# Kernel tuning notes

Hardware: AMD Instinct MI355X
Metric: run time of the kernel (lower is better)

Reference implementation:

```python
import jax, jax.numpy as jnp
import numpy as np

B, V, S, E, K, FF = 16, 512, 1024, 8, 2, 2048  # batch, n_vars, seq_len, n_experts, top_k, ff_dim


def setup_inputs() -> dict:
    key = jax.random.key(0)
    ks = jax.random.split(key, 6)
    def w(k, shape, fan_in):
        return (jax.random.normal(k, shape, jnp.float32) / np.sqrt(fan_in)).astype(jnp.float32)
    return {
        "x": jax.random.normal(ks[0], (B, S, V), jnp.float32),
        "gate_W": w(ks[1], (E, S), S),          # Gating: Linear(seq_len -> n_experts), no bias
        "exp_W": w(ks[2], (E, S, S), S),        # per-expert Linear(seq_len -> seq_len) weights
        "exp_b": jnp.zeros((E, S), jnp.float32),
        "fc1_W": w(ks[3], (FF, V), V),          # MLPFeat fc1: Linear(n_vars -> ff_dim)
        "fc1_b": jnp.zeros((FF,), jnp.float32),
        "fc2_W": w(ks[4], (V, FF), FF),         # MLPFeat fc2: Linear(ff_dim -> n_vars)
        "fc2_b": jnp.zeros((V,), jnp.float32),
    }


def reference(x, gate_W, exp_W, exp_b, fc1_W, fc1_b, fc2_W, fc2_b):
    # Dropout layers are identity at inference.
    res = x                                   # [B,S,V]
    xt = jnp.swapaxes(x, 1, 2)                # [B,V,S] tokens of dim seq_len

    # --- MLPTime (multi_expert MoE) ---
    logits = jnp.einsum('bvs,es->bve', xt, gate_W)      # [B,V,E]
    probs = jax.nn.softmax(logits, axis=-1)             # gate_logits returned by torch code
    w, sel = jax.lax.top_k(probs, K)                    # [B,V,K]
    # combine top-k weights into a dense per-expert weight [B,V,E] (zeros off top-k)
    full_w = jnp.sum(jax.nn.one_hot(sel, E, dtype=xt.dtype) * w[..., None], axis=2)
    # all-expert outputs, then weighted combine (same math as the per-expert scatter loop)
    all_out = jnp.einsum('bvs,eos->bveo', xt, exp_W) + exp_b[None, None]  # [B,V,E,S]
    moe = jnp.einsum('bve,bveo->bvo', full_w, all_out)                    # [B,V,S]
    t = jax.nn.relu(moe)

    x = jnp.swapaxes(t, 1, 2) + res           # [B,S,V] residual

    # --- MLPFeat ---
    res2 = x
    h = jax.nn.relu(x @ fc1_W.T + fc1_b)      # [B,S,FF]
    x = h @ fc2_W.T + fc2_b + res2            # [B,S,V]
    return (x, probs)
```

## Files before the change

kernel.cpp:

```cpp
#include <hip/hip_runtime.h>
#include <stdint.h>

#define B_  16
#define V_  512
#define S_  1024
#define E_  8
#define FF_ 2048
#define NT_ (B_*V_)
#define NR_ (B_*S_)

typedef __attribute__((ext_vector_type(8))) short bf16x8;
typedef __attribute__((ext_vector_type(4))) float f32x4;

__device__ __forceinline__ unsigned short f2bf(float f) {
    unsigned int u = __float_as_uint(f);
    u += 0x7FFFu + ((u >> 16) & 1u);
    return (unsigned short)(u >> 16);
}
__device__ __forceinline__ float bf2f(unsigned short u) {
    return __uint_as_float(((unsigned int)u) << 16);
}

__device__ __forceinline__ void gl_lds16(const void* g, void* l) {
    __builtin_amdgcn_global_load_lds((const __attribute__((address_space(1))) void*)g,
                                     (__attribute__((address_space(3))) void*)l,
                                     16, 0, 0);
}

__device__ __forceinline__ void cvt4(const float* s, unsigned short* d, int i) {
    float4 v = *(const float4*)(s + i);
    ushort4 o; o.x = f2bf(v.x); o.y = f2bf(v.y); o.z = f2bf(v.z); o.w = f2bf(v.w);
    *(ushort4*)(d + i) = o;
}
__global__ void k_convert3(const float* __restrict__ s0, unsigned short* __restrict__ d0, int g0,
                           const float* __restrict__ s1, unsigned short* __restrict__ d1, int g1,
                           const float* __restrict__ s2, unsigned short* __restrict__ d2) {
    int g = blockIdx.x * 256 + threadIdx.x;
    if (g < g0)           cvt4(s0, d0, g * 4);
    else if (g < g0 + g1) cvt4(s1, d1, (g - g0) * 4);
    else                  cvt4(s2, d2, (g - g0 - g1) * 4);
}

__global__ __launch_bounds__(256) void k_xt_gate(const float* __restrict__ x,
                                                 const float* __restrict__ gate_W,
                                                 unsigned short* __restrict__ xt,
                                                 double* __restrict__ part,
                                                 int* __restrict__ cnt) {
    __shared__ float t[32][33];
    __shared__ float gw[E_][128];
    int b = blockIdx.z, sc = blockIdx.y, vt = blockIdx.x;
    int tid = threadIdx.x;
    if (vt == 0 && sc == 0 && b == 0 && tid < E_) cnt[tid] = 0;
    int col = tid & 31, row8 = tid >> 5;
    for (int i = tid; i < E_ * 128; i += 256) {
        int e = i >> 7, j = i & 127;
        gw[e][j] = gate_W[e * S_ + sc * 128 + j];
    }
    double acc = 0.0;
    for (int sub = 0; sub < 4; ++sub) {
        int s0 = sc * 128 + sub * 32;
        __syncthreads();
        for (int r = 0; r < 4; ++r) {
            int sl = row8 + r * 8;
            t[sl][col] = x[(b * S_ + s0 + sl) * V_ + vt * 32 + col];
        }
        __syncthreads();
        for (int r = 0; r < 4; ++r) {
            int vl = row8 + r * 8;
            xt[(size_t)(b * V_ + vt * 32 + vl) * S_ + s0 + col] = f2bf(t[col][vl]);
        }
        #pragma unroll
        for (int s = 0; s < 32; ++s)
            acc += (double)t[s][col] * (double)gw[row8][sub * 32 + s];
    }
    int tok = b * V_ + vt * 32 + col;
    part[((size_t)sc * NT_ + tok) * E_ + row8] = acc;
}

__global__ __launch_bounds__(256) void k_gate_fin(const double* __restrict__ part,
                                                  float* __restrict__ probs_out,
                                                  int* __restrict__ cnt, int* __restrict__ tok_of,
                                                  int* __restrict__ tk_slot, float* __restrict__ tk_w) {
    int t = blockIdx.x * 256 + threadIdx.x;
    int lane = threadIdx.x & 63;
    double l[E_];
    #pragma unroll
    for (int e = 0; e < E_; ++e) l[e] = 0.0;
    for (int c = 0; c < S_ / 128; ++c) {
        const double* p = part + ((size_t)c * NT_ + t) * E_;
        #pragma unroll
        for (int e = 0; e < E_; ++e) l[e] += p[e];
    }
    double m = l[0];
    #pragma unroll
    for (int e = 1; e < E_; ++e) m = l[e] > m ? l[e] : m;
    double p[E_], sum = 0.0;
    #pragma unroll
    for (int e = 0; e < E_; ++e) { p[e] = exp(l[e] - m); sum += p[e]; }
    float pf[E_];
    #pragma unroll
    for (int e = 0; e < E_; ++e) pf[e] = (float)(p[e] / sum);
    float4 pa = {pf[0], pf[1], pf[2], pf[3]}, pb = {pf[4], pf[5], pf[6], pf[7]};
    *(float4*)(probs_out + (size_t)t * E_) = pa;
    *(float4*)(probs_out + (size_t)t * E_ + 4) = pb;
    int i0 = 0;
    #pragma unroll
    for (int e = 1; e < E_; ++e) if (pf[e] > pf[i0]) i0 = e;
    int i1 = -1;
    #pragma unroll
    for (int e = 0; e < E_; ++e) if (e != i0 && (i1 < 0 || pf[e] > pf[i1])) i1 = e;
    int sel[2] = {i0, i1};
    float wsel[2] = {pf[i0], pf[i1]};
    #pragma unroll
    for (int k = 0; k < 2; ++k) {
        int ie = sel[k];
        int pos = 0;
        for (int e = 0; e < E_; ++e) {
            unsigned long long msk = __ballot(ie == e);
            if (ie == e) {
                int rank = __popcll(msk & ((1ull << lane) - 1ull));
                int leader = __ffsll((long long)msk) - 1;
                int base = 0;
                if (lane == leader) base = atomicAdd(&cnt[e], __popcll(msk));
                base = __shfl(base, leader);
                pos = base + rank;
            }
        }
        tok_of[ie * NT_ + pos] = t;
        tk_slot[t * 2 + k] = (ie << 16) | pos;
        tk_w[t * 2 + k] = wsel[k];
    }
}

__device__ __forceinline__ void stage8(const unsigned short* (&ap)[4],
                                       const unsigned short* (&bp)[4],
                                       char* ldsA, char* ldsB, int kt, int wave) {
    const int off = kt * 64;
    char* la = ldsA + wave * 4096;
    char* lb = ldsB + wave * 4096;
    gl_lds16(ap[0] + off, la);
    gl_lds16(ap[1] + off, la + 1024);
    gl_lds16(ap[2] + off, la + 2048);
    gl_lds16(ap[3] + off, la + 3072);
    gl_lds16(bp[0] + off, lb);
    gl_lds16(bp[1] + off, lb + 1024);
    gl_lds16(bp[2] + off, lb + 2048);
    gl_lds16(bp[3] + off, lb + 3072);
}

template<bool LAST>
__device__ __forceinline__ void body64(const short* As, const short* Bs,
                                       int wmBase, int wnBase, int lr, int pb,
                                       f32x4 (&acc)[8][4]) {
    if (LAST) asm volatile("s_waitcnt vmcnt(0)" ::: "memory");
    else      asm volatile("s_waitcnt vmcnt(8)" ::: "memory");
    __builtin_amdgcn_s_barrier();
    __builtin_amdgcn_sched_barrier(0);
    bf16x8 bfv[4][2];
    #pragma unroll
    for (int j = 0; j < 4; ++j)
        #pragma unroll
        for (int ks = 0; ks < 2; ++ks)
            bfv[j][ks] = *(const bf16x8*)(Bs + (wnBase + j * 16 + lr) * 64 + (pb ^ (ks << 5)));
    #pragma unroll
    for (int q = 0; q < 4; ++q) {
        bf16x8 af[2][2];
        #pragma unroll
        for (int f = 0; f < 2; ++f)
            #pragma unroll
            for (int ks = 0; ks < 2; ++ks)
                af[f][ks] = *(const bf16x8*)(As + (wmBase + q * 32 + f * 16 + lr) * 64 + (pb ^ (ks << 5)));
        __builtin_amdgcn_s_barrier();
        __builtin_amdgcn_s_setprio(1);
        #pragma unroll
        for (int f = 0; f < 2; ++f)
            #pragma unroll
            for (int j = 0; j < 4; ++j)
                #pragma unroll
                for (int ks = 0; ks < 2; ++ks)
                    acc[q * 2 + f][j] = __builtin_amdgcn_mfma_f32_16x16x32_bf16(
                        af[f][ks], bfv[j][ks], acc[q * 2 + f][j], 0, 0, 0);
        __builtin_amdgcn_s_setprio(0);
        __builtin_amdgcn_s_barrier();
    }
}

template<int KT>
__device__ __forceinline__ void gemm8(const unsigned short* (&ap)[4],
                                      const unsigned short* (&bp)[4],
                                      char* smem, int wave, int lane,
                                      f32x4 (&acc)[8][4]) {
    char* A0 = smem;           char* B0 = smem + 32768;
    char* A1 = smem + 65536;   char* B1 = smem + 98304;
    const int wmBase = (wave >> 2) * 128;
    const int wnBase = (wave & 3) * 64;
    const int lr = lane & 15;
    const int pb = ((lane >> 4) ^ (lr & 7)) * 8;
    stage8(ap, bp, A0, B0, 0, wave);
    stage8(ap, bp, A1, B1, 1, wave);
    for (int kt = 0; kt + 2 < KT; kt += 2) {
        body64<false>((const short*)A0, (const short*)B0, wmBase, wnBase, lr, pb, acc);
        stage8(ap, bp, A0, B0, kt + 2, wave);
        body64<false>((const short*)A1, (const short*)B1, wmBase, wnBase, lr, pb, acc);
        stage8(ap, bp, A1, B1, kt + 3, wave);
    }
    body64<false>((const short*)A0, (const short*)B0, wmBase, wnBase, lr, pb, acc);
    body64<true >((const short*)A1, (const short*)B1, wmBase, wnBase, lr, pb, acc);
}

__global__ __launch_bounds__(512, 1) void k_moe_gemm8(const unsigned short* __restrict__ xt,
                                                      const unsigned short* __restrict__ expWb,
                                                      const float* __restrict__ exp_b,
                                                      const int* __restrict__ cnt,
                                                      const int* __restrict__ tok_of,
                                                      unsigned short* __restrict__ Yb) {
    int bx = ((int)(blockIdx.x & 7)) * 9 + (int)(blockIdx.x >> 3);
    int e = -1, pos0 = 0, yrow0 = 0, ne = 0;
    {
        int tb = 0, o = 0;
        #pragma unroll
        for (int i = 0; i < E_; ++i) {
            int ci = cnt[i];
            int nti = (ci + 255) >> 8;
            if (e < 0 && bx < tb + nti) { e = i; pos0 = (bx - tb) * 256; yrow0 = o; ne = ci; }
            tb += nti; o += ci;
        }
    }
    if (e < 0) return;
    int nt = blockIdx.y;
    extern __shared__ char smem[];
    int tid = threadIdx.x, wave = tid >> 6, lane = tid & 63;
    int rowLoc = wave * 32 + (lane >> 3);
    int cg = ((lane & 7) ^ ((lane >> 3) & 7)) * 8;
    const unsigned short* Wb = expWb + (size_t)e * S_ * S_;
    const unsigned short* ap[4];
    const unsigned short* bp[4];
    #pragma unroll
    for (int c = 0; c < 4; ++c) {
        int rr = rowLoc + c * 8;
        int tok = tok_of[e * NT_ + min(pos0 + rr, ne - 1)];
        ap[c] = xt + (size_t)tok * S_ + cg;
        bp[c] = Wb + (size_t)(nt * 256 + rr) * S_ + cg;
    }
    f32x4 acc[8][4] = {};
    gemm8<S_ / 64>(ap, bp, smem, wave, lane, acc);
    int wmBase = (wave >> 2) * 128, wnBase = (wave & 3) * 64;
    int lr = lane & 15, quad = lane >> 4;
    #pragma unroll
    for (int i = 0; i < 8; ++i)
        #pragma unroll
        for (int r = 0; r < 4; ++r) {
            int pos = pos0 + wmBase + i * 16 + quad * 4 + r;
            if (pos < ne) {
                size_t row = (size_t)(yrow0 + pos);
                #pragma unroll
                for (int j = 0; j < 4; ++j) {
                    int col = nt * 256 + wnBase + j * 16 + lr;
                    Yb[row * S_ + col] = f2bf(acc[i][j][r] + exp_b[e * S_ + col]);
                }
            }
        }
}

__global__ __launch_bounds__(512, 1) void k_fc1_8p(const unsigned short* __restrict__ x2b,
                                                   const unsigned short* __restrict__ w1b,
                                                   const float* __restrict__ fc1_b,
                                                   unsigned short* __restrict__ h) {
    extern __shared__ char smem[];
    int tid = threadIdx.x, wave = tid >> 6, lane = tid & 63;
    int m0 = blockIdx.x * 256, n0 = blockIdx.y * 256;
    int rowLoc = wave * 32 + (lane >> 3);
    int cg = ((lane & 7) ^ ((lane >> 3) & 7)) * 8;
    const unsigned short* ap[4];
    const unsigned short* bp[4];
    #pragma unroll
    for (int c = 0; c < 4; ++c) {
        int rr = rowLoc + c * 8;
        ap[c] = x2b + (size_t)(m0 + rr) * V_ + cg;
        bp[c] = w1b + (size_t)(n0 + rr) * V_ + cg;
    }
    f32x4 acc[8][4] = {};
    gemm8<V_ / 64>(ap, bp, smem, wave, lane, acc);
    int wmBase = (wave >> 2) * 128, wnBase = (wave & 3) * 64;
    int lr = lane & 15, quad = lane >> 4;
    #pragma unroll
    for (int i = 0; i < 8; ++i)
        #pragma unroll
        for (int r = 0; r < 4; ++r) {
            size_t row = (size_t)(m0 + wmBase + i * 16 + quad * 4 + r);
            #pragma unroll
            for (int j = 0; j < 4; ++j) {
                int col = n0 + wnBase + j * 16 + lr;
                h[row * FF_ + col] = f2bf(fmaxf(acc[i][j][r] + fc1_b[col], 0.f));
            }
        }
}

__device__ __forceinline__ void gemm_k_loop64(const unsigned short* (&ap)[4],
                                              const unsigned short* (&bp)[4],
                                              short* As, short* Bs, int kIters, int wave, int lane,
                                              f32x4 (&acc)[4][4]) {
    char* ldsA = (char*)As + wave * 4096;
    char* ldsB = (char*)Bs + wave * 4096;
    int wm = (wave & 1) << 6, wn = (wave >> 1) << 6;
    int lr = lane & 15, quad = lane >> 4;
    int pb = (quad ^ (lr & 7)) * 8;
    const unsigned short* a0 = ap[0]; const unsigned short* a1 = ap[1];
    const unsigned short* a2 = ap[2]; const unsigned short* a3 = ap[3];
    const unsigned short* b0 = bp[0]; const unsigned short* b1 = bp[1];
    const unsigned short* b2 = bp[2]; const unsigned short* b3 = bp[3];
    for (int kk = 0; kk < kIters; ++kk) {
        gl_lds16(a0, ldsA);        gl_lds16(a1, ldsA + 1024);
        gl_lds16(a2, ldsA + 2048); gl_lds16(a3, ldsA + 3072);
        gl_lds16(b0, ldsB);        gl_lds16(b1, ldsB + 1024);
        gl_lds16(b2, ldsB + 2048); gl_lds16(b3, ldsB + 3072);
        a0 += 64; a1 += 64; a2 += 64; a3 += 64;
        b0 += 64; b1 += 64; b2 += 64; b3 += 64;
        __syncthreads();
        #pragma unroll
        for (int ks = 0; ks < 2; ++ks) {
            int po = pb ^ (ks << 5);
            bf16x8 af[4], bfv[4];
            #pragma unroll
            for (int i = 0; i < 4; ++i)
                af[i] = *(const bf16x8*)(As + (wm + i * 16 + lr) * 64 + po);
            #pragma unroll
            for (int j = 0; j < 4; ++j)
                bfv[j] = *(const bf16x8*)(Bs + (wn + j * 16 + lr) * 64 + po);
            #pragma unroll
            for (int i = 0; i < 4; ++i)
                #pragma unroll
                for (int j = 0; j < 4; ++j)
                    acc[i][j] = __builtin_amdgcn_mfma_f32_16x16x32_bf16(af[i], bfv[j], acc[i][j], 0, 0, 0);
        }
        __syncthreads();
    }
}

__global__ void k_combine(const float* __restrict__ x, const unsigned short* __restrict__ Yb,
                          const int* __restrict__ cnt, const int* __restrict__ tk_slot,
                          const float* __restrict__ tk_w,
                          unsigned short* __restrict__ x2b) {
    __shared__ float t[32][33];
    int b = blockIdx.z, st = blockIdx.y, vt = blockIdx.x;
    int tid = threadIdx.x;
    int vl = tid >> 3, sq = (tid & 7) * 4;
    int tok = b * V_ + vt * 32 + vl;
    int s0 = tk_slot[tok * 2 + 0], s1 = tk_slot[tok * 2 + 1];
    float w0 = tk_w[tok * 2 + 0], w1 = tk_w[tok * 2 + 1];
    int e0 = s0 >> 16, e1 = s1 >> 16;
    int r0b = 0, r1b = 0, o = 0;
    #pragma unroll
    for (int i = 0; i < E_; ++i) {
        if (i == e0) r0b = o;
        if (i == e1) r1b = o;
        o += cnt[i];
    }
    size_t r0 = (size_t)(r0b + (s0 & 0xFFFF));
    size_t r1 = (size_t)(r1b + (s1 & 0xFFFF));
    int sg = st * 32 + sq;
    ushort4 y0 = *(const ushort4*)(Yb + r0 * S_ + sg);
    ushort4 y1 = *(const ushort4*)(Yb + r1 * S_ + sg);
    t[vl][sq + 0] = fmaxf(w0 * bf2f(y0.x) + w1 * bf2f(y1.x), 0.f);
    t[vl][sq + 1] = fmaxf(w0 * bf2f(y0.y) + w1 * bf2f(y1.y), 0.f);
    t[vl][sq + 2] = fmaxf(w0 * bf2f(y0.z) + w1 * bf2f(y1.z), 0.f);
    t[vl][sq + 3] = fmaxf(w0 * bf2f(y0.w) + w1 * bf2f(y1.w), 0.f);
    __syncthreads();
    int vcol = tid & 31, srow8 = tid >> 5;
    for (int r = 0; r < 4; ++r) {
        int sl = srow8 + r * 8;
        size_t gi = (size_t)(b * S_ + st * 32 + sl) * V_ + vt * 32 + vcol;
        x2b[gi] = f2bf(x[gi] + t[vcol][sl]);
    }
}

__global__ __launch_bounds__(256, 3) void k_fc2(const unsigned short* __restrict__ h,
                                                const unsigned short* __restrict__ w2b,
                                                const float* __restrict__ fc2_b,
                                                const unsigned short* __restrict__ x2b,
                                                float* __restrict__ out) {
    __shared__ __align__(16) short As[128 * 64];
    __shared__ __align__(16) short Bs[128 * 64];
    int tid = threadIdx.x, wave = tid >> 6, lane = tid & 63;
    int rowLoc = wave * 32 + (lane >> 3);
    int cg = ((lane & 7) ^ ((lane >> 3) & 7)) * 8;
    int m0 = blockIdx.x * 128, n0 = blockIdx.y * 128;
    const unsigned short* ap[4];
    const unsigned short* bp[4];
    #pragma unroll
    for (int c = 0; c < 4; ++c) {
        int rr = rowLoc + c * 8;
        ap[c] = h + (size_t)(m0 + rr) * FF_ + cg;
        bp[c] = w2b + (size_t)(n0 + rr) * FF_ + cg;
    }
    f32x4 acc[4][4] = {};
    gemm_k_loop64(ap, bp, As, Bs, FF_ / 64, wave, lane, acc);
    int wm = (wave & 1) << 6, wn = (wave >> 1) << 6;
    int lr = lane & 15, quad = lane >> 4;
    #pragma unroll
    for (int i = 0; i < 4; ++i)
        #pragma unroll
        for (int r = 0; r < 4; ++r) {
            size_t row = (size_t)(m0 + wm + i * 16 + quad * 4 + r);
            #pragma unroll
            for (int j = 0; j < 4; ++j) {
                int col = n0 + wn + j * 16 + lr;
                out[row * V_ + col] = acc[i][j][r] + fc2_b[col] + bf2f(x2b[row * V_ + col]);
            }
        }
}

extern "C" void kernel_launch(void* const* d_in, const int* in_sizes, int n_in,
                              void* d_out, int out_size, void* d_ws, size_t ws_size,
                              hipStream_t stream) {
    const float* x      = (const float*)d_in[0];
    const float* gate_W = (const float*)d_in[1];
    const float* exp_W  = (const float*)d_in[2];
    const float* exp_b  = (const float*)d_in[3];
    const float* fc1_W  = (const float*)d_in[4];
    const float* fc1_b  = (const float*)d_in[5];
    const float* fc2_W  = (const float*)d_in[6];
    const float* fc2_b  = (const float*)d_in[7];
    float* out_x = (float*)d_out;
    float* out_p = (float*)d_out + (size_t)B_ * S_ * V_;

    if (ws_size < (size_t)155582592) return;

    char* ws = (char*)d_ws;
    unsigned short* Yb    = (unsigned short*)(ws);
    unsigned short* xt    = (unsigned short*)(ws +  67108864);
    unsigned short* x2b   = (unsigned short*)(ws + 117440512);
    unsigned short* expWb = (unsigned short*)(ws + 134217728);
    unsigned short* fc1Wb = (unsigned short*)(ws + 150994944);
    unsigned short* fc2Wb = (unsigned short*)(ws + 153092096);
    char* route = ws + 155189248;
    int*   cnt     = (int*)(route);
    int*   tok_of  = (int*)(route + 128);
    int*   tk_slot = (int*)(route + 128 + 262144);
    float* tk_w    = (float*)(route + 128 + 262144 + 65536);
    unsigned short* h = (unsigned short*)ws;
    double* part = (double*)ws;

    k_convert3<<<dim3((2097152 + 262144 + 262144) / 256), 256, 0, stream>>>(
        exp_W, expWb, 2097152, fc1_W, fc1Wb, 262144, fc2_W, fc2Wb);
    k_xt_gate<<<dim3(V_ / 32, S_ / 128, B_), 256, 0, stream>>>(x, gate_W, xt, part, cnt);
    k_gate_fin<<<dim3(NT_ / 256), 256, 0, stream>>>(part, out_p, cnt, tok_of, tk_slot, tk_w);
    k_moe_gemm8<<<dim3(72, S_ / 256), 512, 131072, stream>>>(xt, expWb, exp_b, cnt, tok_of, Yb);
    k_combine<<<dim3(V_ / 32, S_ / 32, B_), 256, 0, stream>>>(x, Yb, cnt, tk_slot, tk_w, x2b);
    k_fc1_8p<<<dim3(NR_ / 256, FF_ / 256), 512, 131072, stream>>>(x2b, fc1Wb, fc1_b, h);
    k_fc2<<<dim3(NR_ / 128, V_ / 128), 256, 0, stream>>>(h, fc2Wb, fc2_b, x2b, out_x);
}
```

Before: 330.8 us.

## Fuse weight conversion into gate prep and shrink MoE GEMM tiles to 128x128

```diff
diff --git a/kernel.cpp b/kernel.cpp
--- a/kernel.cpp
+++ b/kernel.cpp
@@ -32,24 +32,29 @@
     ushort4 o; o.x = f2bf(v.x); o.y = f2bf(v.y); o.z = f2bf(v.z); o.w = f2bf(v.w);
     *(ushort4*)(d + i) = o;
 }
-__global__ void k_convert3(const float* __restrict__ s0, unsigned short* __restrict__ d0, int g0,
-                           const float* __restrict__ s1, unsigned short* __restrict__ d1, int g1,
-                           const float* __restrict__ s2, unsigned short* __restrict__ d2) {
-    int g = blockIdx.x * 256 + threadIdx.x;
-    if (g < g0)           cvt4(s0, d0, g * 4);
-    else if (g < g0 + g1) cvt4(s1, d1, (g - g0) * 4);
-    else                  cvt4(s2, d2, (g - g0 - g1) * 4);
-}
-
-__global__ __launch_bounds__(256) void k_xt_gate(const float* __restrict__ x,
-                                                 const float* __restrict__ gate_W,
-                                                 unsigned short* __restrict__ xt,
-                                                 double* __restrict__ part,
-                                                 int* __restrict__ cnt) {
+__global__ __launch_bounds__(256) void k_prep(const float* __restrict__ x,
+                                              const float* __restrict__ gate_W,
+                                              unsigned short* __restrict__ xt,
+                                              double* __restrict__ part,
+                                              int* __restrict__ cnt,
+                                              const float* __restrict__ expW, unsigned short* __restrict__ expWb,
+                                              const float* __restrict__ fc1W, unsigned short* __restrict__ fc1Wb,
+                                              const float* __restrict__ fc2W, unsigned short* __restrict__ fc2Wb) {
+    int tid = threadIdx.x;
+    if (blockIdx.z >= 16) {
+        int cid = ((int)blockIdx.z - 16) * 128 + (int)blockIdx.y * 16 + (int)blockIdx.x;
+        #pragma unroll
+        for (int rep = 0; rep < 2; ++rep) {
+            int g = (cid + rep * 5120) * 256 + tid;
+            if (g < 2097152)              cvt4(expW, expWb, g * 4);
+            else if (g < 2097152 + 262144) cvt4(fc1W, fc1Wb, (g - 2097152) * 4);
+            else                           cvt4(fc2W, fc2Wb, (g - 2097152 - 262144) * 4);
+        }
+        return;
+    }
     __shared__ float t[32][33];
     __shared__ float gw[E_][128];
     int b = blockIdx.z, sc = blockIdx.y, vt = blockIdx.x;
-    int tid = threadIdx.x;
     if (vt == 0 && sc == 0 && b == 0 && tid < E_) cnt[tid] = 0;
     int col = tid & 31, row8 = tid >> 5;
     for (int i = tid; i < E_ * 128; i += 256) {
@@ -130,170 +135,6 @@
         tk_slot[t * 2 + k] = (ie << 16) | pos;
         tk_w[t * 2 + k] = wsel[k];
     }
-}
-
-__device__ __forceinline__ void stage8(const unsigned short* (&ap)[4],
-                                       const unsigned short* (&bp)[4],
-                                       char* ldsA, char* ldsB, int kt, int wave) {
-    const int off = kt * 64;
-    char* la = ldsA + wave * 4096;
-    char* lb = ldsB + wave * 4096;
-    gl_lds16(ap[0] + off, la);
-    gl_lds16(ap[1] + off, la + 1024);
-    gl_lds16(ap[2] + off, la + 2048);
-    gl_lds16(ap[3] + off, la + 3072);
-    gl_lds16(bp[0] + off, lb);
-    gl_lds16(bp[1] + off, lb + 1024);
-    gl_lds16(bp[2] + off, lb + 2048);
-    gl_lds16(bp[3] + off, lb + 3072);
-}
-
-template<bool LAST>
-__device__ __forceinline__ void body64(const short* As, const short* Bs,
-                                       int wmBase, int wnBase, int lr, int pb,
-                                       f32x4 (&acc)[8][4]) {
-    if (LAST) asm volatile("s_waitcnt vmcnt(0)" ::: "memory");
-    else      asm volatile("s_waitcnt vmcnt(8)" ::: "memory");
-    __builtin_amdgcn_s_barrier();
-    __builtin_amdgcn_sched_barrier(0);
-    bf16x8 bfv[4][2];
-    #pragma unroll
-    for (int j = 0; j < 4; ++j)
-        #pragma unroll
-        for (int ks = 0; ks < 2; ++ks)
-            bfv[j][ks] = *(const bf16x8*)(Bs + (wnBase + j * 16 + lr) * 64 + (pb ^ (ks << 5)));
-    #pragma unroll
-    for (int q = 0; q < 4; ++q) {
-        bf16x8 af[2][2];
-        #pragma unroll
-        for (int f = 0; f < 2; ++f)
-            #pragma unroll
-            for (int ks = 0; ks < 2; ++ks)
-                af[f][ks] = *(const bf16x8*)(As + (wmBase + q * 32 + f * 16 + lr) * 64 + (pb ^ (ks << 5)));
-        __builtin_amdgcn_s_barrier();
-        __builtin_amdgcn_s_setprio(1);
-        #pragma unroll
-        for (int f = 0; f < 2; ++f)
-            #pragma unroll
-            for (int j = 0; j < 4; ++j)
-                #pragma unroll
-                for (int ks = 0; ks < 2; ++ks)
-                    acc[q * 2 + f][j] = __builtin_amdgcn_mfma_f32_16x16x32_bf16(
-                        af[f][ks], bfv[j][ks], acc[q * 2 + f][j], 0, 0, 0);
-        __builtin_amdgcn_s_setprio(0);
-        __builtin_amdgcn_s_barrier();
-    }
-}
-
-template<int KT>
-__device__ __forceinline__ void gemm8(const unsigned short* (&ap)[4],
-                                      const unsigned short* (&bp)[4],
-                                      char* smem, int wave, int lane,
-                                      f32x4 (&acc)[8][4]) {
-    char* A0 = smem;           char* B0 = smem + 32768;
-    char* A1 = smem + 65536;   char* B1 = smem + 98304;
-    const int wmBase = (wave >> 2) * 128;
-    const int wnBase = (wave & 3) * 64;
-    const int lr = lane & 15;
-    const int pb = ((lane >> 4) ^ (lr & 7)) * 8;
-    stage8(ap, bp, A0, B0, 0, wave);
-    stage8(ap, bp, A1, B1, 1, wave);
-    for (int kt = 0; kt + 2 < KT; kt += 2) {
-        body64<false>((const short*)A0, (const short*)B0, wmBase, wnBase, lr, pb, acc);
-        stage8(ap, bp, A0, B0, kt + 2, wave);
-        body64<false>((const short*)A1, (const short*)B1, wmBase, wnBase, lr, pb, acc);
-        stage8(ap, bp, A1, B1, kt + 3, wave);
-    }
-    body64<false>((const short*)A0, (const short*)B0, wmBase, wnBase, lr, pb, acc);
-    body64<true >((const short*)A1, (const short*)B1, wmBase, wnBase, lr, pb, acc);
-}
-
-__global__ __launch_bounds__(512, 1) void k_moe_gemm8(const unsigned short* __restrict__ xt,
-                                                      const unsigned short* __restrict__ expWb,
-                                                      const float* __restrict__ exp_b,
-                                                      const int* __restrict__ cnt,
-                                                      const int* __restrict__ tok_of,
-                                                      unsigned short* __restrict__ Yb) {
-    int bx = ((int)(blockIdx.x & 7)) * 9 + (int)(blockIdx.x >> 3);
-    int e = -1, pos0 = 0, yrow0 = 0, ne = 0;
-    {
-        int tb = 0, o = 0;
-        #pragma unroll
-        for (int i = 0; i < E_; ++i) {
-            int ci = cnt[i];
-            int nti = (ci + 255) >> 8;
-            if (e < 0 && bx < tb + nti) { e = i; pos0 = (bx - tb) * 256; yrow0 = o; ne = ci; }
-            tb += nti; o += ci;
-        }
-    }
-    if (e < 0) return;
-    int nt = blockIdx.y;
-    extern __shared__ char smem[];
-    int tid = threadIdx.x, wave = tid >> 6, lane = tid & 63;
-    int rowLoc = wave * 32 + (lane >> 3);
-    int cg = ((lane & 7) ^ ((lane >> 3) & 7)) * 8;
-    const unsigned short* Wb = expWb + (size_t)e * S_ * S_;
-    const unsigned short* ap[4];
-    const unsigned short* bp[4];
-    #pragma unroll
-    for (int c = 0; c < 4; ++c) {
-        int rr = rowLoc + c * 8;
-        int tok = tok_of[e * NT_ + min(pos0 + rr, ne - 1)];
-        ap[c] = xt + (size_t)tok * S_ + cg;
-        bp[c] = Wb + (size_t)(nt * 256 + rr) * S_ + cg;
-    }
-    f32x4 acc[8][4] = {};
-    gemm8<S_ / 64>(ap, bp, smem, wave, lane, acc);
-    int wmBase = (wave >> 2) * 128, wnBase = (wave & 3) * 64;
-    int lr = lane & 15, quad = lane >> 4;
-    #pragma unroll
-    for (int i = 0; i < 8; ++i)
-        #pragma unroll
-        for (int r = 0; r < 4; ++r) {
-            int pos = pos0 + wmBase + i * 16 + quad * 4 + r;
-            if (pos < ne) {
-                size_t row = (size_t)(yrow0 + pos);
-                #pragma unroll
-                for (int j = 0; j < 4; ++j) {
-                    int col = nt * 256 + wnBase + j * 16 + lr;
-                    Yb[row * S_ + col] = f2bf(acc[i][j][r] + exp_b[e * S_ + col]);
-                }
-            }
-        }
-}
-
-__global__ __launch_bounds__(512, 1) void k_fc1_8p(const unsigned short* __restrict__ x2b,
-                                                   const unsigned short* __restrict__ w1b,
-                                                   const float* __restrict__ fc1_b,
-                                                   unsigned short* __restrict__ h) {
-    extern __shared__ char smem[];
-    int tid = threadIdx.x, wave = tid >> 6, lane = tid & 63;
-    int m0 = blockIdx.x * 256, n0 = blockIdx.y * 256;
-    int rowLoc = wave * 32 + (lane >> 3);
-    int cg = ((lane & 7) ^ ((lane >> 3) & 7)) * 8;
-    const unsigned short* ap[4];
-    const unsigned short* bp[4];
-    #pragma unroll
-    for (int c = 0; c < 4; ++c) {
-        int rr = rowLoc + c * 8;
-        ap[c] = x2b + (size_t)(m0 + rr) * V_ + cg;
-        bp[c] = w1b + (size_t)(n0 + rr) * V_ + cg;
-    }
-    f32x4 acc[8][4] = {};
-    gemm8<V_ / 64>(ap, bp, smem, wave, lane, acc);
-    int wmBase = (wave >> 2) * 128, wnBase = (wave & 3) * 64;
-    int lr = lane & 15, quad = lane >> 4;
-    #pragma unroll
-    for (int i = 0; i < 8; ++i)
-        #pragma unroll
-        for (int r = 0; r < 4; ++r) {
-            size_t row = (size_t)(m0 + wmBase + i * 16 + quad * 4 + r);
-            #pragma unroll
-            for (int j = 0; j < 4; ++j) {
-                int col = n0 + wnBase + j * 16 + lr;
-                h[row * FF_ + col] = f2bf(fmaxf(acc[i][j][r] + fc1_b[col], 0.f));
-            }
-        }
 }
 
 __device__ __forceinline__ void gemm_k_loop64(const unsigned short* (&ap)[4],
@@ -337,6 +178,61 @@
     }
 }
 
+__global__ __launch_bounds__(256, 3) void k_moe_gemm(const unsigned short* __restrict__ xt,
+                                                     const unsigned short* __restrict__ expWb,
+                                                     const float* __restrict__ exp_b,
+                                                     const int* __restrict__ cnt,
+                                                     const int* __restrict__ tok_of,
+                                                     unsigned short* __restrict__ Yb) {
+    int bx = ((int)(blockIdx.x & 7)) * 17 + (int)(blockIdx.x >> 3);
+    int e = -1, pos0 = 0, yrow0 = 0, ne = 0;
+    {
+        int tb = 0, o = 0;
+        #pragma unroll
+        for (int i = 0; i < E_; ++i) {
+            int ci = cnt[i];
+            int nti = (ci + 127) >> 7;
+            if (e < 0 && bx < tb + nti) { e = i; pos0 = (bx - tb) * 128; yrow0 = o; ne = ci; }
+            tb += nti; o += ci;
+        }
+    }
+    if (e < 0) return;
+    int nt = blockIdx.y;
+    __shared__ __align__(16) short As[128 * 64];
+    __shared__ __align__(16) short Bs[128 * 64];
+    int tid = threadIdx.x, wave = tid >> 6, lane = tid & 63;
+    int rowLoc = wave * 32 + (lane >> 3);
+    int cg = ((lane & 7) ^ ((lane >> 3) & 7)) * 8;
+    const unsigned short* Wb = expWb + (size_t)e * S_ * S_;
+    const unsigned short* ap[4];
+    const unsigned short* bp[4];
+    #pragma unroll
+    for (int c = 0; c < 4; ++c) {
+        int rr = rowLoc + c * 8;
+        int tok = tok_of[e * NT_ + min(pos0 + rr, ne - 1)];
+        ap[c] = xt + (size_t)tok * S_ + cg;
+        bp[c] = Wb + (size_t)(nt * 128 + rr) * S_ + cg;
+    }
+    f32x4 acc[4][4] = {};
+    gemm_k_loop64(ap, bp, As, Bs, S_ / 64, wave, lane, acc);
+    int wm = (wave & 1) << 6, wn = (wave >> 1) << 6;
+    int lr = lane & 15, quad = lane >> 4;
+    #pragma unroll
+    for (int i = 0; i < 4; ++i)
+        #pragma unroll
+        for (int r = 0; r < 4; ++r) {
+            int pos = pos0 + wm + i * 16 + quad * 4 + r;
+            if (pos < ne) {
+                size_t row = (size_t)(yrow0 + pos);
+                #pragma unroll
+                for (int j = 0; j < 4; ++j) {
+                    int col = nt * 128 + wn + j * 16 + lr;
+                    Yb[row * S_ + col] = f2bf(acc[i][j][r] + exp_b[e * S_ + col]);
+                }
+            }
+        }
+}
+
 __global__ void k_combine(const float* __restrict__ x, const unsigned short* __restrict__ Yb,
                           const int* __restrict__ cnt, const int* __restrict__ tk_slot,
                           const float* __restrict__ tk_w,
@@ -374,6 +270,116 @@
     }
 }
 
+__device__ __forceinline__ void stage8(const unsigned short* (&ap)[4],
+                                       const unsigned short* (&bp)[4],
+                                       char* ldsA, char* ldsB, int kt, int wave) {
+    const int off = kt * 64;
+    char* la = ldsA + wave * 4096;
+    char* lb = ldsB + wave * 4096;
+    gl_lds16(ap[0] + off, la);
+    gl_lds16(ap[1] + off, la + 1024);
+    gl_lds16(ap[2] + off, la + 2048);
+    gl_lds16(ap[3] + off, la + 3072);
+    gl_lds16(bp[0] + off, lb);
+    gl_lds16(bp[1] + off, lb + 1024);
+    gl_lds16(bp[2] + off, lb + 2048);
+    gl_lds16(bp[3] + off, lb + 3072);
+}
+
+template<bool LAST>
+__device__ __forceinline__ void body64(const short* As, const short* Bs,
+                                       int wmBase, int wnBase, int lr, int pb,
+                                       f32x4 (&acc)[8][4]) {
+    if (LAST) asm volatile("s_waitcnt vmcnt(0)" ::: "memory");
+    else      asm volatile("s_waitcnt vmcnt(8)" ::: "memory");
+    __builtin_amdgcn_s_barrier();
+    __builtin_amdgcn_sched_barrier(0);
+    bf16x8 bfv[4][2];
+    #pragma unroll
+    for (int j = 0; j < 4; ++j)
+        #pragma unroll
+        for (int ks = 0; ks < 2; ++ks)
+            bfv[j][ks] = *(const bf16x8*)(Bs + (wnBase + j * 16 + lr) * 64 + (pb ^ (ks << 5)));
+    #pragma unroll
+    for (int q = 0; q < 4; ++q) {
+        bf16x8 af[2][2];
+        #pragma unroll
+        for (int f = 0; f < 2; ++f)
+            #pragma unroll
+            for (int ks = 0; ks < 2; ++ks)
+                af[f][ks] = *(const bf16x8*)(As + (wmBase + q * 32 + f * 16 + lr) * 64 + (pb ^ (ks << 5)));
+        __builtin_amdgcn_s_barrier();
+        __builtin_amdgcn_s_setprio(1);
+        #pragma unroll
+        for (int f = 0; f < 2; ++f)
+            #pragma unroll
+            for (int j = 0; j < 4; ++j)
+                #pragma unroll
+                for (int ks = 0; ks < 2; ++ks)
+                    acc[q * 2 + f][j] = __builtin_amdgcn_mfma_f32_16x16x32_bf16(
+                        af[f][ks], bfv[j][ks], acc[q * 2 + f][j], 0, 0, 0);
+        __builtin_amdgcn_s_setprio(0);
+        __builtin_amdgcn_s_barrier();
+    }
+}
+
+template<int KT>
+__device__ __forceinline__ void gemm8(const unsigned short* (&ap)[4],
+                                      const unsigned short* (&bp)[4],
+                                      char* smem, int wave, int lane,
+                                      f32x4 (&acc)[8][4]) {
+    char* A0 = smem;           char* B0 = smem + 32768;
+    char* A1 = smem + 65536;   char* B1 = smem + 98304;
+    const int wmBase = (wave >> 2) * 128;
+    const int wnBase = (wave & 3) * 64;
+    const int lr = lane & 15;
+    const int pb = ((lane >> 4) ^ (lr & 7)) * 8;
+    stage8(ap, bp, A0, B0, 0, wave);
+    stage8(ap, bp, A1, B1, 1, wave);
+    for (int kt = 0; kt + 2 < KT; kt += 2) {
+        body64<false>((const short*)A0, (const short*)B0, wmBase, wnBase, lr, pb, acc);
+        stage8(ap, bp, A0, B0, kt + 2, wave);
+        body64<false>((const short*)A1, (const short*)B1, wmBase, wnBase, lr, pb, acc);
+        stage8(ap, bp, A1, B1, kt + 3, wave);
+    }
+    body64<false>((const short*)A0, (const short*)B0, wmBase, wnBase, lr, pb, acc);
+    body64<true >((const short*)A1, (const short*)B1, wmBase, wnBase, lr, pb, acc);
+}
+
+__global__ __launch_bounds__(512, 1) void k_fc1_8p(const unsigned short* __restrict__ x2b,
+                                                   const unsigned short* __restrict__ w1b,
+                                                   const float* __restrict__ fc1_b,
+                                                   unsigned short* __restrict__ h) {
+    extern __shared__ char smem[];
+    int tid = threadIdx.x, wave = tid >> 6, lane = tid & 63;
+    int m0 = blockIdx.x * 256, n0 = blockIdx.y * 256;
+    int rowLoc = wave * 32 + (lane >> 3);
+    int cg = ((lane & 7) ^ ((lane >> 3) & 7)) * 8;
+    const unsigned short* ap[4];
+    const unsigned short* bp[4];
+    #pragma unroll
+    for (int c = 0; c < 4; ++c) {
+        int rr = rowLoc + c * 8;
+        ap[c] = x2b + (size_t)(m0 + rr) * V_ + cg;
+        bp[c] = w1b + (size_t)(n0 + rr) * V_ + cg;
+    }
+    f32x4 acc[8][4] = {};
+    gemm8<V_ / 64>(ap, bp, smem, wave, lane, acc);
+    int wmBase = (wave >> 2) * 128, wnBase = (wave & 3) * 64;
+    int lr = lane & 15, quad = lane >> 4;
+    #pragma unroll
+    for (int i = 0; i < 8; ++i)
+        #pragma unroll
+        for (int r = 0; r < 4; ++r) {
+            size_t row = (size_t)(m0 + wmBase + i * 16 + quad * 4 + r);
+            #pragma unroll
+            for (int j = 0; j < 4; ++j) {
+                int col = n0 + wnBase + j * 16 + lr;
+                h[row * FF_ + col] = f2bf(fmaxf(acc[i][j][r] + fc1_b[col], 0.f));
+            }
+        }
+}
+
 __global__ __launch_bounds__(256, 3) void k_fc2(const unsigned short* __restrict__ h,
                                                 const unsigned short* __restrict__ w2b,
                                                 const float* __restrict__ fc2_b,
@@ -441,11 +447,10 @@
     unsigned short* h = (unsigned short*)ws;
     double* part = (double*)ws;
 
-    k_convert3<<<dim3((2097152 + 262144 + 262144) / 256), 256, 0, stream>>>(
-        exp_W, expWb, 2097152, fc1_W, fc1Wb, 262144, fc2_W, fc2Wb);
-    k_xt_gate<<<dim3(V_ / 32, S_ / 128, B_), 256, 0, stream>>>(x, gate_W, xt, part, cnt);
+    k_prep<<<dim3(16, 8, 16 + 40), 256, 0, stream>>>(x, gate_W, xt, part, cnt,
+                                                     exp_W, expWb, fc1_W, fc1Wb, fc2_W, fc2Wb);
     k_gate_fin<<<dim3(NT_ / 256), 256, 0, stream>>>(part, out_p, cnt, tok_of, tk_slot, tk_w);
-    k_moe_gemm8<<<dim3(72, S_ / 256), 512, 131072, stream>>>(xt, expWb, exp_b, cnt, tok_of, Yb);
+    k_moe_gemm<<<dim3(136, S_ / 128), 256, 0, stream>>>(xt, expWb, exp_b, cnt, tok_of, Yb);
     k_combine<<<dim3(V_ / 32, S_ / 32, B_), 256, 0, stream>>>(x, Yb, cnt, tk_slot, tk_w, x2b);
     k_fc1_8p<<<dim3(NR_ / 256, FF_ / 256), 512, 131072, stream>>>(x2b, fc1Wb, fc1_b, h);
     k_fc2<<<dim3(NR_ / 128, V_ / 128), 256, 0, stream>>>(h, fc2Wb, fc2_b, x2b, out_x);
```

New measurement: 306.0 us. -7.5%, faster.
